# Kernel optimization log

Measured on AMD Instinct MI355X. Metric: run time of the kernel, lower is better.

Reference implementation:

```python
import jax, jax.numpy as jnp
import numpy as np

N_NODES = 100000

def gcn_conv(x, W, b, src, dst, n_nodes):
    # PyG GCNConv: out = D^{-1/2} (A + I) D^{-1/2} (x W) + b, deg includes self-loop
    h = x @ W  # [N, H]
    ones = jnp.ones(src.shape[0], dtype=x.dtype)
    deg = jax.ops.segment_sum(ones, dst, num_segments=n_nodes) + 1.0  # +1 self-loop
    dinv = jax.lax.rsqrt(deg)  # deg >= 1, no zeros
    norm = dinv[src] * dinv[dst]  # [E]
    msg = h[src] * norm[:, None]  # [E, H] gather + scale
    agg = jax.ops.segment_sum(msg, dst, num_segments=n_nodes)  # scatter-add
    self_contrib = h * (dinv * dinv)[:, None]  # self-loop term norm = dinv_i^2
    return agg + self_contrib + b


def setup_inputs() -> dict:
    key = jax.random.key(0)
    ks = jax.random.split(key, 6)
    F_IN, H, E = 128, 128, 1600000
    x = jax.random.normal(ks[0], (N_NODES, F_IN), dtype=jnp.float32)
    edge_index = jax.random.randint(ks[1], (2, E), 0, N_NODES, dtype=jnp.int32)
    s = 1.0 / np.sqrt(F_IN)
    W1 = jax.random.normal(ks[2], (F_IN, H), dtype=jnp.float32) * s
    b1 = jnp.zeros((H,), dtype=jnp.float32)
    W2 = jax.random.normal(ks[3], (H, H), dtype=jnp.float32) * (1.0 / np.sqrt(H))
    b2 = jnp.zeros((H,), dtype=jnp.float32)
    Wlin = jax.random.normal(ks[4], (H, 1), dtype=jnp.float32) * (1.0 / np.sqrt(H))
    blin = jnp.zeros((1,), dtype=jnp.float32)
    return {"x": x, "edge_index": edge_index, "W1": W1, "b1": b1,
            "W2": W2, "b2": b2, "Wlin": Wlin, "blin": blin}


def reference(x, edge_index, W1, b1, W2, b2, Wlin, blin):
    src, dst = edge_index[0], edge_index[1]
    h = gcn_conv(x, W1, b1, src, dst, N_NODES)
    h = jax.nn.relu(h)
    h = gcn_conv(h, W2, b2, src, dst, N_NODES)
    h = jax.nn.relu(h)
    out = h @ Wlin + blin  # [N, 1]
    return out.squeeze(-1)  # [N]
```

## Files before the change

kernel.cpp:

```cpp
#include <hip/hip_runtime.h>
#include <hip/hip_fp16.h>

#define NFEAT 128

typedef _Float16 v8hf __attribute__((ext_vector_type(8)));
typedef float v4f __attribute__((ext_vector_type(4)));

__global__ void k_deg_rank(const int* __restrict__ dst, int* __restrict__ deg,
                           int* __restrict__ rank, int E) {
  int e = blockIdx.x * blockDim.x + threadIdx.x;
  if (e < E) rank[e] = atomicAdd(&deg[dst[e]], 1);
}

__global__ void k_prep_w(const float* __restrict__ W1, const float* __restrict__ W2,
                         _Float16* __restrict__ Wt1, _Float16* __restrict__ Wt2) {
  int idx = blockIdx.x * 256 + threadIdx.x;
  const float* W = (idx < 16384) ? W1 : W2;
  _Float16* Wt = (idx < 16384) ? Wt1 : Wt2;
  int i = idx & 16383;
  int k = i >> 7, n = i & 127;
  Wt[n * 128 + k] = (_Float16)W[k * 128 + n];
}

__global__ __launch_bounds__(1024) void k_scan_blocks(const int* __restrict__ deg,
    int* __restrict__ base, int* __restrict__ partials, int n) {
  __shared__ int buf[1024];
  int tid = threadIdx.x;
  int i = blockIdx.x * 1024 + tid;
  int v = (i < n) ? deg[i] : 0;
  buf[tid] = v;
  __syncthreads();
  #pragma unroll
  for (int off = 1; off < 1024; off <<= 1) {
    int t = (tid >= off) ? buf[tid - off] : 0;
    __syncthreads();
    buf[tid] += t;
    __syncthreads();
  }
  if (i < n) base[i] = buf[tid] - v;
  if (tid == 1023) partials[blockIdx.x] = buf[tid];
}

__global__ void k_scan_partials(int* __restrict__ partials, int nb) {
  __shared__ int buf[128];
  int tid = threadIdx.x;
  int v = (tid < nb) ? partials[tid] : 0;
  buf[tid] = v;
  __syncthreads();
  #pragma unroll
  for (int off = 1; off < 128; off <<= 1) {
    int t = (tid >= off) ? buf[tid - off] : 0;
    __syncthreads();
    buf[tid] += t;
    __syncthreads();
  }
  if (tid < nb) partials[tid] = buf[tid] - v;
}

__global__ void k_finalize_base(int* __restrict__ base, const int* __restrict__ partials,
    const int* __restrict__ deg, float* __restrict__ dinv, int n, int E) {
  int i = blockIdx.x * blockDim.x + threadIdx.x;
  if (i < n) {
    base[i] += partials[i >> 10];
    dinv[i] = rsqrtf((float)(deg[i] + 1));
  } else if (i == n) {
    base[n] = E;
  }
}

__global__ void k_scatter(const int* __restrict__ src, const int* __restrict__ dst,
    const int* __restrict__ rank, const int* __restrict__ base,
    int* __restrict__ ssrc, int E) {
  int e = blockIdx.x * blockDim.x + threadIdx.x;
  if (e < E) ssrc[base[dst[e]] + rank[e]] = src[e];
}

template <typename AT>
__global__ __launch_bounds__(256) void k_gemm_mfma(
    const AT* __restrict__ A, const _Float16* __restrict__ Wt,
    const float* __restrict__ dinv, _Float16* __restrict__ g16, int N) {
  __shared__ _Float16 As[64][136];
  __shared__ _Float16 Ws[128][136];
  const int tid = threadIdx.x;
  const int row0 = blockIdx.x * 64;

  if constexpr (sizeof(AT) == 4) {
    #pragma unroll
    for (int i = 0; i < 8; i++) {
      int idx = tid + i * 256;
      int row = idx >> 5;
      int c4 = idx & 31;
      int gr = row0 + row; gr = (gr < N) ? gr : (N - 1);
      float4 v = *(const float4*)((const float*)A + (size_t)gr * NFEAT + c4 * 4);
      _Float16* p = &As[row][c4 * 4];
      p[0] = (_Float16)v.x; p[1] = (_Float16)v.y;
      p[2] = (_Float16)v.z; p[3] = (_Float16)v.w;
    }
  } else {
    #pragma unroll
    for (int i = 0; i < 4; i++) {
      int idx = tid + i * 256;
      int row = idx >> 4;
      int c8 = idx & 15;
      int gr = row0 + row; gr = (gr < N) ? gr : (N - 1);
      *(uint4*)&As[row][c8 * 8] =
          *(const uint4*)((const _Float16*)A + (size_t)gr * NFEAT + c8 * 8);
    }
  }
  #pragma unroll
  for (int i = 0; i < 8; i++) {
    int idx = tid + i * 256;
    int row = idx >> 4;
    int c8 = idx & 15;
    *(uint4*)&Ws[row][c8 * 8] = *(const uint4*)(Wt + (size_t)row * 128 + c8 * 8);
  }
  __syncthreads();

  const int wv = tid >> 6;
  const int lane = tid & 63;
  const int m = lane & 15;
  const int q = lane >> 4;

  v4f acc[8] = {};
  const _Float16* arow = &As[wv * 16 + m][0];
  #pragma unroll
  for (int kt = 0; kt < 4; kt++) {
    v8hf af = *(const v8hf*)(arow + kt * 32 + q * 8);
    #pragma unroll
    for (int ct = 0; ct < 8; ct++) {
      v8hf bf = *(const v8hf*)(&Ws[ct * 16 + m][kt * 32 + q * 8]);
      acc[ct] = __builtin_amdgcn_mfma_f32_16x16x32_f16(af, bf, acc[ct], 0, 0, 0);
    }
  }

  int nd[4]; float dv[4];
  #pragma unroll
  for (int r = 0; r < 4; r++) {
    nd[r] = row0 + wv * 16 + q * 4 + r;
    int c = (nd[r] < N) ? nd[r] : (N - 1);
    dv[r] = dinv[c];
  }
  #pragma unroll
  for (int ct = 0; ct < 8; ct++)
    #pragma unroll
    for (int r = 0; r < 4; r++)
      if (nd[r] < N)
        g16[((size_t)ct * N + nd[r]) * 16 + m] = (_Float16)(acc[ct][r] * dv[r]);
}

__global__ __launch_bounds__(256) void k_agg_slice(
    const __half2* __restrict__ g16, const float* __restrict__ dinv,
    const int* __restrict__ base, const int* __restrict__ ssrc,
    const float* __restrict__ bias, __half2* __restrict__ hB, int N) {
  const int lane = threadIdx.x & 63;
  const int wv = threadIdx.x >> 6;
  const int s = blockIdx.x & 7;
  const int p = lane >> 3, d = lane & 7;
  const int n = (blockIdx.x >> 3) * 32 + wv * 8 + p;
  const bool act = (n < N);
  const int nc = act ? n : (N - 1);
  const __half2* table = g16 + (size_t)s * N * 8;

  float2 acc = __half22float2(table[(size_t)nc * 8 + d]);
  int e = base[nc], b1 = base[nc + 1];
  if (!act) { e = 0; b1 = 0; }
  for (; e + 4 <= b1; e += 4) {
    int s0 = ssrc[e], s1 = ssrc[e + 1], s2 = ssrc[e + 2], s3 = ssrc[e + 3];
    float2 f0 = __half22float2(table[(size_t)s0 * 8 + d]);
    float2 f1 = __half22float2(table[(size_t)s1 * 8 + d]);
    float2 f2 = __half22float2(table[(size_t)s2 * 8 + d]);
    float2 f3 = __half22float2(table[(size_t)s3 * 8 + d]);
    acc.x += (f0.x + f1.x) + (f2.x + f3.x);
    acc.y += (f0.y + f1.y) + (f2.y + f3.y);
  }
  for (; e < b1; ++e) {
    float2 f = __half22float2(table[(size_t)ssrc[e] * 8 + d]);
    acc.x += f.x; acc.y += f.y;
  }
  if (act) {
    float dvn = dinv[n];
    float2 bb = *(const float2*)(bias + s * 16 + d * 2);
    hB[(size_t)n * 64 + s * 8 + d] =
        __floats2half2_rn(fmaxf(acc.x * dvn + bb.x, 0.f),
                          fmaxf(acc.y * dvn + bb.y, 0.f));
  }
}

__global__ __launch_bounds__(256) void k_agg_final_slice(
    const __half2* __restrict__ g16, const float* __restrict__ dinv,
    const int* __restrict__ base, const int* __restrict__ ssrc,
    const float* __restrict__ bias, const float* __restrict__ wlin,
    const float* __restrict__ blin, float* __restrict__ out, int N) {
  const int lane = threadIdx.x & 63;
  const int wv = threadIdx.x >> 6;
  const int s = blockIdx.x & 7;
  const int p = lane >> 3, d = lane & 7;
  const int n = (blockIdx.x >> 3) * 32 + wv * 8 + p;
  const bool act = (n < N);
  const int nc = act ? n : (N - 1);
  const __half2* table = g16 + (size_t)s * N * 8;

  float2 acc = __half22float2(table[(size_t)nc * 8 + d]);
  int e = base[nc], b1 = base[nc + 1];
  if (!act) { e = 0; b1 = 0; }
  for (; e + 4 <= b1; e += 4) {
    int s0 = ssrc[e], s1 = ssrc[e + 1], s2 = ssrc[e + 2], s3 = ssrc[e + 3];
    float2 f0 = __half22float2(table[(size_t)s0 * 8 + d]);
    float2 f1 = __half22float2(table[(size_t)s1 * 8 + d]);
    float2 f2 = __half22float2(table[(size_t)s2 * 8 + d]);
    float2 f3 = __half22float2(table[(size_t)s3 * 8 + d]);
    acc.x += (f0.x + f1.x) + (f2.x + f3.x);
    acc.y += (f0.y + f1.y) + (f2.y + f3.y);
  }
  for (; e < b1; ++e) {
    float2 f = __half22float2(table[(size_t)ssrc[e] * 8 + d]);
    acc.x += f.x; acc.y += f.y;
  }
  if (act) {
    float dvn = dinv[n];
    float2 bb = *(const float2*)(bias + s * 16 + d * 2);
    float2 wl = *(const float2*)(wlin + s * 16 + d * 2);
    float pv = fmaxf(acc.x * dvn + bb.x, 0.f) * wl.x +
               fmaxf(acc.y * dvn + bb.y, 0.f) * wl.y;
    #pragma unroll
    for (int m = 1; m <= 4; m <<= 1) pv += __shfl_xor(pv, m, 64);
    if (d == 0) atomicAdd(out + n, pv + (s == 0 ? blin[0] : 0.f));
  }
}

extern "C" void kernel_launch(void* const* d_in, const int* in_sizes, int n_in,
                              void* d_out, int out_size, void* d_ws, size_t ws_size,
                              hipStream_t stream) {
  const float* x    = (const float*)d_in[0];
  const int*   ei   = (const int*)d_in[1];
  const float* W1   = (const float*)d_in[2];
  const float* b1   = (const float*)d_in[3];
  const float* W2   = (const float*)d_in[4];
  const float* b2   = (const float*)d_in[5];
  const float* Wlin = (const float*)d_in[6];
  const float* blin = (const float*)d_in[7];
  const int N = in_sizes[0] / NFEAT;
  const int E = in_sizes[1] / 2;
  const int* src = ei;
  const int* dst = ei + E;

  int* ws_i = (int*)d_ws;
  size_t off = 0;
  int* deg      = ws_i + off; off += N;
  int* base     = ws_i + off; off += (size_t)N + 1;
  off = (off + 3) & ~(size_t)3;
  int* partials = ws_i + off; off += 128;
  int* ssrc     = ws_i + off; off += E;
  float* dinv   = (float*)(ws_i + off); off += N;
  off = (off + 3) & ~(size_t)3;
  _Float16* Wt1 = (_Float16*)(ws_i + off); off += 8192;
  _Float16* Wt2 = (_Float16*)(ws_i + off); off += 8192;
  _Float16* g16 = (_Float16*)(ws_i + off); off += (size_t)N * 64;
  _Float16* hB  = (_Float16*)(ws_i + off); off += (size_t)N * 64;
  int* rank     = (int*)g16;

  hipMemsetAsync(deg, 0, (size_t)N * sizeof(int), stream);
  hipMemsetAsync(d_out, 0, (size_t)N * sizeof(float), stream);

  const int tpbE = 256;
  const int gE = (E + tpbE - 1) / tpbE;
  k_deg_rank<<<gE, tpbE, 0, stream>>>(dst, deg, rank, E);
  k_prep_w<<<128, 256, 0, stream>>>(W1, W2, Wt1, Wt2);

  const int nb = (N + 1023) / 1024;
  k_scan_blocks<<<nb, 1024, 0, stream>>>(deg, base, partials, N);
  k_scan_partials<<<1, 128, 0, stream>>>(partials, nb);
  k_finalize_base<<<((N + 1) + 255) / 256, 256, 0, stream>>>(base, partials, deg, dinv, N, E);
  k_scatter<<<gE, tpbE, 0, stream>>>(src, dst, rank, base, ssrc, E);

  const int gg = (N + 63) / 64;
  const int ga = 8 * ((N + 31) / 32);
  k_gemm_mfma<float><<<gg, 256, 0, stream>>>(x, Wt1, dinv, g16, N);
  k_agg_slice<<<ga, 256, 0, stream>>>((const __half2*)g16, dinv, base, ssrc, b1,
                                      (__half2*)hB, N);
  k_gemm_mfma<_Float16><<<gg, 256, 0, stream>>>(hB, Wt2, dinv, g16, N);
  k_agg_final_slice<<<ga, 256, 0, stream>>>((const __half2*)g16, dinv, base, ssrc, b2,
                                            Wlin, blin, (float*)d_out, N);
}
```

Before: 431.6 us.

## Pad CSR rows to multiples of 8 with dummy zero-row indices for vectorized gather

Rounds each node's CSR segment length up to a multiple of 8 and fills the padding with index N, which points at an added all-zero row in each feature slice of the gathered table. The aggregation kernels then load neighbor indices as int4 pairs and run an 8-wide unrolled loop with two accumulators, with no remainder loop. This is meant to cut per-edge index load instructions and tail handling and to raise memory-level parallelism. In exchange it adds a fill pass over the padded index array and wasted gathers of the zero row, about 3.5 extra entries per node on average.

New measurement: 426.2 us. No clear change (-1.3%).

```diff
diff --git a/kernel.cpp b/kernel.cpp
--- a/kernel.cpp
+++ b/kernel.cpp
@@ -10,6 +10,11 @@
                            int* __restrict__ rank, int E) {
   int e = blockIdx.x * blockDim.x + threadIdx.x;
   if (e < E) rank[e] = atomicAdd(&deg[dst[e]], 1);
+}
+
+__global__ void k_fill(int* __restrict__ p, int v, int n) {
+  int i = blockIdx.x * 256 + threadIdx.x;
+  if (i < n) p[i] = v;
 }
 
 __global__ void k_prep_w(const float* __restrict__ W1, const float* __restrict__ W2,
@@ -27,7 +32,7 @@
   __shared__ int buf[1024];
   int tid = threadIdx.x;
   int i = blockIdx.x * 1024 + tid;
-  int v = (i < n) ? deg[i] : 0;
+  int v = (i < n) ? ((deg[i] + 7) & ~7) : 0;
   buf[tid] = v;
   __syncthreads();
   #pragma unroll
@@ -37,7 +42,7 @@
     buf[tid] += t;
     __syncthreads();
   }
-  if (i < n) base[i] = buf[tid] - v;
+  if (i <= n) base[i] = buf[tid] - v;
   if (tid == 1023) partials[blockIdx.x] = buf[tid];
 }
 
@@ -58,13 +63,11 @@
 }
 
 __global__ void k_finalize_base(int* __restrict__ base, const int* __restrict__ partials,
-    const int* __restrict__ deg, float* __restrict__ dinv, int n, int E) {
+    const int* __restrict__ deg, float* __restrict__ dinv, int n) {
   int i = blockIdx.x * blockDim.x + threadIdx.x;
-  if (i < n) {
+  if (i <= n) {
     base[i] += partials[i >> 10];
-    dinv[i] = rsqrtf((float)(deg[i] + 1));
-  } else if (i == n) {
-    base[n] = E;
+    if (i < n) dinv[i] = rsqrtf((float)(deg[i] + 1));
   }
 }
 
@@ -73,6 +76,12 @@
     int* __restrict__ ssrc, int E) {
   int e = blockIdx.x * blockDim.x + threadIdx.x;
   if (e < E) ssrc[base[dst[e]] + rank[e]] = src[e];
+}
+
+__global__ void k_zero_row(_Float16* __restrict__ g16, int N) {
+  int i = threadIdx.x;
+  int s = i >> 4, m = i & 15;
+  g16[((size_t)s * (N + 1) + N) * 16 + m] = (_Float16)0.f;
 }
 
 template <typename AT>
@@ -145,7 +154,7 @@
     #pragma unroll
     for (int r = 0; r < 4; r++)
       if (nd[r] < N)
-        g16[((size_t)ct * N + nd[r]) * 16 + m] = (_Float16)(acc[ct][r] * dv[r]);
+        g16[((size_t)ct * (N + 1) + nd[r]) * 16 + m] = (_Float16)(acc[ct][r] * dv[r]);
 }
 
 __global__ __launch_bounds__(256) void k_agg_slice(
@@ -159,30 +168,34 @@
   const int n = (blockIdx.x >> 3) * 32 + wv * 8 + p;
   const bool act = (n < N);
   const int nc = act ? n : (N - 1);
-  const __half2* table = g16 + (size_t)s * N * 8;
-
-  float2 acc = __half22float2(table[(size_t)nc * 8 + d]);
-  int e = base[nc], b1 = base[nc + 1];
-  if (!act) { e = 0; b1 = 0; }
-  for (; e + 4 <= b1; e += 4) {
-    int s0 = ssrc[e], s1 = ssrc[e + 1], s2 = ssrc[e + 2], s3 = ssrc[e + 3];
-    float2 f0 = __half22float2(table[(size_t)s0 * 8 + d]);
-    float2 f1 = __half22float2(table[(size_t)s1 * 8 + d]);
-    float2 f2 = __half22float2(table[(size_t)s2 * 8 + d]);
-    float2 f3 = __half22float2(table[(size_t)s3 * 8 + d]);
-    acc.x += (f0.x + f1.x) + (f2.x + f3.x);
-    acc.y += (f0.y + f1.y) + (f2.y + f3.y);
-  }
-  for (; e < b1; ++e) {
-    float2 f = __half22float2(table[(size_t)ssrc[e] * 8 + d]);
-    acc.x += f.x; acc.y += f.y;
+  const __half2* table = g16 + (size_t)s * (N + 1) * 8;
+
+  float2 a0 = __half22float2(table[(size_t)nc * 8 + d]);
+  float2 a1 = make_float2(0.f, 0.f);
+  int e = base[nc], b1e = base[nc + 1];
+  if (!act) b1e = e;
+  for (; e < b1e; e += 8) {
+    int4 ia = *(const int4*)(ssrc + e);
+    int4 ib = *(const int4*)(ssrc + e + 4);
+    float2 f0 = __half22float2(table[(size_t)ia.x * 8 + d]);
+    float2 f1 = __half22float2(table[(size_t)ia.y * 8 + d]);
+    float2 f2 = __half22float2(table[(size_t)ia.z * 8 + d]);
+    float2 f3 = __half22float2(table[(size_t)ia.w * 8 + d]);
+    float2 f4 = __half22float2(table[(size_t)ib.x * 8 + d]);
+    float2 f5 = __half22float2(table[(size_t)ib.y * 8 + d]);
+    float2 f6 = __half22float2(table[(size_t)ib.z * 8 + d]);
+    float2 f7 = __half22float2(table[(size_t)ib.w * 8 + d]);
+    a0.x += (f0.x + f1.x) + (f2.x + f3.x);
+    a0.y += (f0.y + f1.y) + (f2.y + f3.y);
+    a1.x += (f4.x + f5.x) + (f6.x + f7.x);
+    a1.y += (f4.y + f5.y) + (f6.y + f7.y);
   }
   if (act) {
     float dvn = dinv[n];
     float2 bb = *(const float2*)(bias + s * 16 + d * 2);
     hB[(size_t)n * 64 + s * 8 + d] =
-        __floats2half2_rn(fmaxf(acc.x * dvn + bb.x, 0.f),
-                          fmaxf(acc.y * dvn + bb.y, 0.f));
+        __floats2half2_rn(fmaxf((a0.x + a1.x) * dvn + bb.x, 0.f),
+                          fmaxf((a0.y + a1.y) * dvn + bb.y, 0.f));
   }
 }
 
@@ -198,30 +211,34 @@
   const int n = (blockIdx.x >> 3) * 32 + wv * 8 + p;
   const bool act = (n < N);
   const int nc = act ? n : (N - 1);
-  const __half2* table = g16 + (size_t)s * N * 8;
-
-  float2 acc = __half22float2(table[(size_t)nc * 8 + d]);
-  int e = base[nc], b1 = base[nc + 1];
-  if (!act) { e = 0; b1 = 0; }
-  for (; e + 4 <= b1; e += 4) {
-    int s0 = ssrc[e], s1 = ssrc[e + 1], s2 = ssrc[e + 2], s3 = ssrc[e + 3];
-    float2 f0 = __half22float2(table[(size_t)s0 * 8 + d]);
-    float2 f1 = __half22float2(table[(size_t)s1 * 8 + d]);
-    float2 f2 = __half22float2(table[(size_t)s2 * 8 + d]);
-    float2 f3 = __half22float2(table[(size_t)s3 * 8 + d]);
-    acc.x += (f0.x + f1.x) + (f2.x + f3.x);
-    acc.y += (f0.y + f1.y) + (f2.y + f3.y);
-  }
-  for (; e < b1; ++e) {
-    float2 f = __half22float2(table[(size_t)ssrc[e] * 8 + d]);
-    acc.x += f.x; acc.y += f.y;
+  const __half2* table = g16 + (size_t)s * (N + 1) * 8;
+
+  float2 a0 = __half22float2(table[(size_t)nc * 8 + d]);
+  float2 a1 = make_float2(0.f, 0.f);
+  int e = base[nc], b1e = base[nc + 1];
+  if (!act) b1e = e;
+  for (; e < b1e; e += 8) {
+    int4 ia = *(const int4*)(ssrc + e);
+    int4 ib = *(const int4*)(ssrc + e + 4);
+    float2 f0 = __half22float2(table[(size_t)ia.x * 8 + d]);
+    float2 f1 = __half22float2(table[(size_t)ia.y * 8 + d]);
+    float2 f2 = __half22float2(table[(size_t)ia.z * 8 + d]);
+    float2 f3 = __half22float2(table[(size_t)ia.w * 8 + d]);
+    float2 f4 = __half22float2(table[(size_t)ib.x * 8 + d]);
+    float2 f5 = __half22float2(table[(size_t)ib.y * 8 + d]);
+    float2 f6 = __half22float2(table[(size_t)ib.z * 8 + d]);
+    float2 f7 = __half22float2(table[(size_t)ib.w * 8 + d]);
+    a0.x += (f0.x + f1.x) + (f2.x + f3.x);
+    a0.y += (f0.y + f1.y) + (f2.y + f3.y);
+    a1.x += (f4.x + f5.x) + (f6.x + f7.x);
+    a1.y += (f4.y + f5.y) + (f6.y + f7.y);
   }
   if (act) {
     float dvn = dinv[n];
     float2 bb = *(const float2*)(bias + s * 16 + d * 2);
     float2 wl = *(const float2*)(wlin + s * 16 + d * 2);
-    float pv = fmaxf(acc.x * dvn + bb.x, 0.f) * wl.x +
-               fmaxf(acc.y * dvn + bb.y, 0.f) * wl.y;
+    float pv = fmaxf((a0.x + a1.x) * dvn + bb.x, 0.f) * wl.x +
+               fmaxf((a0.y + a1.y) * dvn + bb.y, 0.f) * wl.y;
     #pragma unroll
     for (int m = 1; m <= 4; m <<= 1) pv += __shfl_xor(pv, m, 64);
     if (d == 0) atomicAdd(out + n, pv + (s == 0 ? blin[0] : 0.f));
@@ -243,6 +260,7 @@
   const int E = in_sizes[1] / 2;
   const int* src = ei;
   const int* dst = ei + E;
+  const int Epad = E + 8 * N + 8;
 
   int* ws_i = (int*)d_ws;
   size_t off = 0;
@@ -250,12 +268,12 @@
   int* base     = ws_i + off; off += (size_t)N + 1;
   off = (off + 3) & ~(size_t)3;
   int* partials = ws_i + off; off += 128;
-  int* ssrc     = ws_i + off; off += E;
+  int* ssrc     = ws_i + off; off += Epad;
   float* dinv   = (float*)(ws_i + off); off += N;
   off = (off + 3) & ~(size_t)3;
   _Float16* Wt1 = (_Float16*)(ws_i + off); off += 8192;
   _Float16* Wt2 = (_Float16*)(ws_i + off); off += 8192;
-  _Float16* g16 = (_Float16*)(ws_i + off); off += (size_t)N * 64;
+  _Float16* g16 = (_Float16*)(ws_i + off); off += (size_t)(N + 1) * 64 + 32;
   _Float16* hB  = (_Float16*)(ws_i + off); off += (size_t)N * 64;
   int* rank     = (int*)g16;
 
@@ -265,13 +283,15 @@
   const int tpbE = 256;
   const int gE = (E + tpbE - 1) / tpbE;
   k_deg_rank<<<gE, tpbE, 0, stream>>>(dst, deg, rank, E);
+  k_fill<<<(Epad + 255) / 256, 256, 0, stream>>>(ssrc, N, Epad);
   k_prep_w<<<128, 256, 0, stream>>>(W1, W2, Wt1, Wt2);
 
-  const int nb = (N + 1023) / 1024;
+  const int nb = (N + 1 + 1023) / 1024;
   k_scan_blocks<<<nb, 1024, 0, stream>>>(deg, base, partials, N);
   k_scan_partials<<<1, 128, 0, stream>>>(partials, nb);
-  k_finalize_base<<<((N + 1) + 255) / 256, 256, 0, stream>>>(base, partials, deg, dinv, N, E);
+  k_finalize_base<<<((N + 1) + 255) / 256, 256, 0, stream>>>(base, partials, deg, dinv, N);
   k_scatter<<<gE, tpbE, 0, stream>>>(src, dst, rank, base, ssrc, E);
+  k_zero_row<<<1, 128, 0, stream>>>(g16, N);
 
   const int gg = (N + 63) / 64;
   const int ga = 8 * ((N + 31) / 32);
```

## Use row-major features with wave-per-node aggregation and self-loops folded into CSR

Applied to the files above, without the earlier changes.

The GEMM output moves from a feature-sliced layout (8 slices of 16 features) to row-major [N,128] fp16. Aggregation now gives one wavefront per node covering all 128 features, unrolled by 8 edges, in place of eight slice blocks that each reread the CSR indices. Self-loops become explicit CSR edges, so degree and dinv come directly from the counts. The final layer reduces across the wave and writes out[n] directly, removing the output memset and the atomics. The cost is N extra edges in the sort and scatter passes, with one node per wave and less index reuse, which may lower occupancy on high-degree imbalance.

After: 401.2 us. -7.0%, faster.

```diff
diff --git a/kernel.cpp b/kernel.cpp
--- a/kernel.cpp
+++ b/kernel.cpp
@@ -7,9 +7,10 @@
 typedef float v4f __attribute__((ext_vector_type(4)));
 
 __global__ void k_deg_rank(const int* __restrict__ dst, int* __restrict__ deg,
-                           int* __restrict__ rank, int E) {
+                           int* __restrict__ rank, int E, int N) {
   int e = blockIdx.x * blockDim.x + threadIdx.x;
   if (e < E) rank[e] = atomicAdd(&deg[dst[e]], 1);
+  else if (e < E + N) rank[e] = atomicAdd(&deg[e - E], 1);
 }
 
 __global__ void k_prep_w(const float* __restrict__ W1, const float* __restrict__ W2,
@@ -37,7 +38,7 @@
     buf[tid] += t;
     __syncthreads();
   }
-  if (i < n) base[i] = buf[tid] - v;
+  if (i <= n) base[i] = buf[tid] - v;
   if (tid == 1023) partials[blockIdx.x] = buf[tid];
 }
 
@@ -58,21 +59,20 @@
 }
 
 __global__ void k_finalize_base(int* __restrict__ base, const int* __restrict__ partials,
-    const int* __restrict__ deg, float* __restrict__ dinv, int n, int E) {
+    const int* __restrict__ deg, float* __restrict__ dinv, int n) {
   int i = blockIdx.x * blockDim.x + threadIdx.x;
-  if (i < n) {
+  if (i <= n) {
     base[i] += partials[i >> 10];
-    dinv[i] = rsqrtf((float)(deg[i] + 1));
-  } else if (i == n) {
-    base[n] = E;
+    if (i < n) dinv[i] = rsqrtf((float)deg[i]);
   }
 }
 
 __global__ void k_scatter(const int* __restrict__ src, const int* __restrict__ dst,
     const int* __restrict__ rank, const int* __restrict__ base,
-    int* __restrict__ ssrc, int E) {
+    int* __restrict__ ssrc, int E, int N) {
   int e = blockIdx.x * blockDim.x + threadIdx.x;
   if (e < E) ssrc[base[dst[e]] + rank[e]] = src[e];
+  else if (e < E + N) { int n = e - E; ssrc[base[n] + rank[e]] = n; }
 }
 
 template <typename AT>
@@ -145,87 +145,79 @@
     #pragma unroll
     for (int r = 0; r < 4; r++)
       if (nd[r] < N)
-        g16[((size_t)ct * N + nd[r]) * 16 + m] = (_Float16)(acc[ct][r] * dv[r]);
-}
-
-__global__ __launch_bounds__(256) void k_agg_slice(
-    const __half2* __restrict__ g16, const float* __restrict__ dinv,
+        g16[(size_t)nd[r] * NFEAT + ct * 16 + m] = (_Float16)(acc[ct][r] * dv[r]);
+}
+
+__global__ __launch_bounds__(256) void k_agg(
+    const __half2* __restrict__ g, const float* __restrict__ dinv,
     const int* __restrict__ base, const int* __restrict__ ssrc,
     const float* __restrict__ bias, __half2* __restrict__ hB, int N) {
   const int lane = threadIdx.x & 63;
-  const int wv = threadIdx.x >> 6;
-  const int s = blockIdx.x & 7;
-  const int p = lane >> 3, d = lane & 7;
-  const int n = (blockIdx.x >> 3) * 32 + wv * 8 + p;
-  const bool act = (n < N);
-  const int nc = act ? n : (N - 1);
-  const __half2* table = g16 + (size_t)s * N * 8;
-
-  float2 acc = __half22float2(table[(size_t)nc * 8 + d]);
-  int e = base[nc], b1 = base[nc + 1];
-  if (!act) { e = 0; b1 = 0; }
-  for (; e + 4 <= b1; e += 4) {
-    int s0 = ssrc[e], s1 = ssrc[e + 1], s2 = ssrc[e + 2], s3 = ssrc[e + 3];
-    float2 f0 = __half22float2(table[(size_t)s0 * 8 + d]);
-    float2 f1 = __half22float2(table[(size_t)s1 * 8 + d]);
-    float2 f2 = __half22float2(table[(size_t)s2 * 8 + d]);
-    float2 f3 = __half22float2(table[(size_t)s3 * 8 + d]);
-    acc.x += (f0.x + f1.x) + (f2.x + f3.x);
-    acc.y += (f0.y + f1.y) + (f2.y + f3.y);
+  const int n = blockIdx.x * 4 + (threadIdx.x >> 6);
+  if (n >= N) return;
+  int e = base[n], b1 = base[n + 1];
+  float2 acc = make_float2(0.f, 0.f);
+  for (; e + 8 <= b1; e += 8) {
+    int s0 = ssrc[e],     s1 = ssrc[e + 1], s2 = ssrc[e + 2], s3 = ssrc[e + 3];
+    int s4 = ssrc[e + 4], s5 = ssrc[e + 5], s6 = ssrc[e + 6], s7 = ssrc[e + 7];
+    float2 f0 = __half22float2(g[(size_t)s0 * 64 + lane]);
+    float2 f1 = __half22float2(g[(size_t)s1 * 64 + lane]);
+    float2 f2 = __half22float2(g[(size_t)s2 * 64 + lane]);
+    float2 f3 = __half22float2(g[(size_t)s3 * 64 + lane]);
+    float2 f4 = __half22float2(g[(size_t)s4 * 64 + lane]);
+    float2 f5 = __half22float2(g[(size_t)s5 * 64 + lane]);
+    float2 f6 = __half22float2(g[(size_t)s6 * 64 + lane]);
+    float2 f7 = __half22float2(g[(size_t)s7 * 64 + lane]);
+    acc.x += (f0.x + f1.x) + (f2.x + f3.x) + (f4.x + f5.x) + (f6.x + f7.x);
+    acc.y += (f0.y + f1.y) + (f2.y + f3.y) + (f4.y + f5.y) + (f6.y + f7.y);
   }
   for (; e < b1; ++e) {
-    float2 f = __half22float2(table[(size_t)ssrc[e] * 8 + d]);
+    float2 f = __half22float2(g[(size_t)ssrc[e] * 64 + lane]);
     acc.x += f.x; acc.y += f.y;
   }
-  if (act) {
-    float dvn = dinv[n];
-    float2 bb = *(const float2*)(bias + s * 16 + d * 2);
-    hB[(size_t)n * 64 + s * 8 + d] =
-        __floats2half2_rn(fmaxf(acc.x * dvn + bb.x, 0.f),
-                          fmaxf(acc.y * dvn + bb.y, 0.f));
-  }
-}
-
-__global__ __launch_bounds__(256) void k_agg_final_slice(
-    const __half2* __restrict__ g16, const float* __restrict__ dinv,
+  float dvn = dinv[n];
+  float2 bb = *(const float2*)(bias + lane * 2);
+  hB[(size_t)n * 64 + lane] =
+      __floats2half2_rn(fmaxf(acc.x * dvn + bb.x, 0.f),
+                        fmaxf(acc.y * dvn + bb.y, 0.f));
+}
+
+__global__ __launch_bounds__(256) void k_agg_final(
+    const __half2* __restrict__ g, const float* __restrict__ dinv,
     const int* __restrict__ base, const int* __restrict__ ssrc,
     const float* __restrict__ bias, const float* __restrict__ wlin,
     const float* __restrict__ blin, float* __restrict__ out, int N) {
   const int lane = threadIdx.x & 63;
-  const int wv = threadIdx.x >> 6;
-  const int s = blockIdx.x & 7;
-  const int p = lane >> 3, d = lane & 7;
-  const int n = (blockIdx.x >> 3) * 32 + wv * 8 + p;
-  const bool act = (n < N);
-  const int nc = act ? n : (N - 1);
-  const __half2* table = g16 + (size_t)s * N * 8;
-
-  float2 acc = __half22float2(table[(size_t)nc * 8 + d]);
-  int e = base[nc], b1 = base[nc + 1];
-  if (!act) { e = 0; b1 = 0; }
-  for (; e + 4 <= b1; e += 4) {
-    int s0 = ssrc[e], s1 = ssrc[e + 1], s2 = ssrc[e + 2], s3 = ssrc[e + 3];
-    float2 f0 = __half22float2(table[(size_t)s0 * 8 + d]);
-    float2 f1 = __half22float2(table[(size_t)s1 * 8 + d]);
-    float2 f2 = __half22float2(table[(size_t)s2 * 8 + d]);
-    float2 f3 = __half22float2(table[(size_t)s3 * 8 + d]);
-    acc.x += (f0.x + f1.x) + (f2.x + f3.x);
-    acc.y += (f0.y + f1.y) + (f2.y + f3.y);
+  const int n = blockIdx.x * 4 + (threadIdx.x >> 6);
+  if (n >= N) return;
+  int e = base[n], b1 = base[n + 1];
+  float2 acc = make_float2(0.f, 0.f);
+  for (; e + 8 <= b1; e += 8) {
+    int s0 = ssrc[e],     s1 = ssrc[e + 1], s2 = ssrc[e + 2], s3 = ssrc[e + 3];
+    int s4 = ssrc[e + 4], s5 = ssrc[e + 5], s6 = ssrc[e + 6], s7 = ssrc[e + 7];
+    float2 f0 = __half22float2(g[(size_t)s0 * 64 + lane]);
+    float2 f1 = __half22float2(g[(size_t)s1 * 64 + lane]);
+    float2 f2 = __half22float2(g[(size_t)s2 * 64 + lane]);
+    float2 f3 = __half22float2(g[(size_t)s3 * 64 + lane]);
+    float2 f4 = __half22float2(g[(size_t)s4 * 64 + lane]);
+    float2 f5 = __half22float2(g[(size_t)s5 * 64 + lane]);
+    float2 f6 = __half22float2(g[(size_t)s6 * 64 + lane]);
+    float2 f7 = __half22float2(g[(size_t)s7 * 64 + lane]);
+    acc.x += (f0.x + f1.x) + (f2.x + f3.x) + (f4.x + f5.x) + (f6.x + f7.x);
+    acc.y += (f0.y + f1.y) + (f2.y + f3.y) + (f4.y + f5.y) + (f6.y + f7.y);
   }
   for (; e < b1; ++e) {
-    float2 f = __half22float2(table[(size_t)ssrc[e] * 8 + d]);
+    float2 f = __half22float2(g[(size_t)ssrc[e] * 64 + lane]);
     acc.x += f.x; acc.y += f.y;
   }
-  if (act) {
-    float dvn = dinv[n];
-    float2 bb = *(const float2*)(bias + s * 16 + d * 2);
-    float2 wl = *(const float2*)(wlin + s * 16 + d * 2);
-    float pv = fmaxf(acc.x * dvn + bb.x, 0.f) * wl.x +
-               fmaxf(acc.y * dvn + bb.y, 0.f) * wl.y;
-    #pragma unroll
-    for (int m = 1; m <= 4; m <<= 1) pv += __shfl_xor(pv, m, 64);
-    if (d == 0) atomicAdd(out + n, pv + (s == 0 ? blin[0] : 0.f));
-  }
+  float dvn = dinv[n];
+  float2 bb = *(const float2*)(bias + lane * 2);
+  float2 wl = *(const float2*)(wlin + lane * 2);
+  float pv = fmaxf(acc.x * dvn + bb.x, 0.f) * wl.x +
+             fmaxf(acc.y * dvn + bb.y, 0.f) * wl.y;
+  #pragma unroll
+  for (int off = 32; off >= 1; off >>= 1) pv += __shfl_down(pv, off, 64);
+  if (lane == 0) out[n] = pv + blin[0];
 }
 
 extern "C" void kernel_launch(void* const* d_in, const int* in_sizes, int n_in,
@@ -243,6 +235,7 @@
   const int E = in_sizes[1] / 2;
   const int* src = ei;
   const int* dst = ei + E;
+  const int Etot = E + N;
 
   int* ws_i = (int*)d_ws;
   size_t off = 0;
@@ -250,7 +243,7 @@
   int* base     = ws_i + off; off += (size_t)N + 1;
   off = (off + 3) & ~(size_t)3;
   int* partials = ws_i + off; off += 128;
-  int* ssrc     = ws_i + off; off += E;
+  int* ssrc     = ws_i + off; off += Etot;
   float* dinv   = (float*)(ws_i + off); off += N;
   off = (off + 3) & ~(size_t)3;
   _Float16* Wt1 = (_Float16*)(ws_i + off); off += 8192;
@@ -260,25 +253,24 @@
   int* rank     = (int*)g16;
 
   hipMemsetAsync(deg, 0, (size_t)N * sizeof(int), stream);
-  hipMemsetAsync(d_out, 0, (size_t)N * sizeof(float), stream);
 
   const int tpbE = 256;
-  const int gE = (E + tpbE - 1) / tpbE;
-  k_deg_rank<<<gE, tpbE, 0, stream>>>(dst, deg, rank, E);
+  const int gE = (Etot + tpbE - 1) / tpbE;
+  k_deg_rank<<<gE, tpbE, 0, stream>>>(dst, deg, rank, E, N);
   k_prep_w<<<128, 256, 0, stream>>>(W1, W2, Wt1, Wt2);
 
-  const int nb = (N + 1023) / 1024;
+  const int nb = (N + 1 + 1023) / 1024;
   k_scan_blocks<<<nb, 1024, 0, stream>>>(deg, base, partials, N);
   k_scan_partials<<<1, 128, 0, stream>>>(partials, nb);
-  k_finalize_base<<<((N + 1) + 255) / 256, 256, 0, stream>>>(base, partials, deg, dinv, N, E);
-  k_scatter<<<gE, tpbE, 0, stream>>>(src, dst, rank, base, ssrc, E);
+  k_finalize_base<<<((N + 1) + 255) / 256, 256, 0, stream>>>(base, partials, deg, dinv, N);
+  k_scatter<<<gE, tpbE, 0, stream>>>(src, dst, rank, base, ssrc, E, N);
 
   const int gg = (N + 63) / 64;
-  const int ga = 8 * ((N + 31) / 32);
+  const int ga = (N + 3) / 4;
   k_gemm_mfma<float><<<gg, 256, 0, stream>>>(x, Wt1, dinv, g16, N);
-  k_agg_slice<<<ga, 256, 0, stream>>>((const __half2*)g16, dinv, base, ssrc, b1,
-                                      (__half2*)hB, N);
+  k_agg<<<ga, 256, 0, stream>>>((const __half2*)g16, dinv, base, ssrc, b1,
+                                (__half2*)hB, N);
   k_gemm_mfma<_Float16><<<gg, 256, 0, stream>>>(hB, Wt2, dinv, g16, N);
-  k_agg_final_slice<<<ga, 256, 0, stream>>>((const __half2*)g16, dinv, base, ssrc, b2,
-                                            Wlin, blin, (float*)d_out, N);
-}
+  k_agg_final<<<ga, 256, 0, stream>>>((const __half2*)g16, dinv, base, ssrc, b2,
+                                      Wlin, blin, (float*)d_out, N);
+}
```
